# Kernel optimization log

Hardware: AMD Instinct MI355X
Metric: run time of the kernel (lower is better)

Reference implementation:

```python
import jax, jax.numpy as jnp
import numpy as np


def setup_inputs() -> dict:
    key = jax.random.key(0)
    k1, k2, k3 = jax.random.split(key, 3)
    B, C_in, C_out, T = 16, 512, 512, 4096
    pre = jax.random.normal(k1, (B, C_in, T), dtype=jnp.float32)
    # nn.Linear weight layout: [out_features, in_features]
    W_pre = jax.random.normal(k2, (C_out, C_in), dtype=jnp.float32) * (1.0 / np.sqrt(C_in))
    b_pre = jax.random.normal(k3, (C_out,), dtype=jnp.float32) * 0.01
    return {"pre": pre, "W_pre": W_pre, "b_pre": b_pre}


def reference(pre, W_pre, b_pre):
    # Original 'casual' branch loops over T applying w_pre(_pre[:,:,i]) into BOTH
    # embedding_prev and embedding_curr, then sums -> 2 * (W_pre @ pre + b).
    # Batched form: one einsum over the full sequence.
    y = jnp.einsum('bct,oc->bot', pre, W_pre) + b_pre[None, :, None]  # [B, C_out, T]
    return y + y
```

## Files before the change

### kernel.cpp

```cpp
#include <hip/hip_runtime.h>
#include <hip/hip_bf16.h>

typedef __attribute__((ext_vector_type(8))) short short8_t;
typedef __attribute__((ext_vector_type(4))) float f32x4;

#define BATCH 16
#define CIN   512
#define COUT  512
#define TT    4096
#define BK    128
#define NKT   (CIN / BK)

__device__ __forceinline__ uint pk2(float a, float b) {
    ushort lo = __builtin_bit_cast(ushort, __float2bfloat16(a));
    ushort hi = __builtin_bit_cast(ushort, __float2bfloat16(b));
    return (uint)lo | ((uint)hi << 16);
}

extern "C" __global__ __launch_bounds__(256)
void wconv(const float* __restrict__ W, ushort* __restrict__ Wb)
{
    const int i  = blockIdx.x * 256 + threadIdx.x;
    const int m  = i >> 7;
    const int k0 = (i & 127) * 4;
    const float4 v = *(const float4*)(W + (size_t)m * CIN + k0);
    const int bm = m >> 4, r = m & 15;
    const int ksg = k0 >> 5, g = (k0 >> 3) & 3, k7 = k0 & 7;
    uint2 q;
    q.x = pk2(v.x, v.y);
    q.y = pk2(v.z, v.w);
    *(uint2*)&Wb[(size_t)bm * 8192 + ksg * 512 + g * 128 + r * 8 + k7] = q;
}

template<bool WSB>
__global__ __launch_bounds__(256)
void conv2x1_gemm(const float* __restrict__ pre, const float* __restrict__ W,
                  const ushort* __restrict__ Wb,
                  const float* __restrict__ bias, float* __restrict__ out)
{
    __shared__ alignas(16) ushort LB[2][16 * 512];

    const int tid  = threadIdx.x;
    const int lane = tid & 63;
    const int wm   = tid >> 6;
    const int g    = lane >> 4;
    const int l15  = lane & 15;

    const int id   = ((blockIdx.x & 7) << 9) | (blockIdx.x >> 3);
    const int mblk = id & 3;
    const int ti   = (id >> 2) & 63;
    const int bb   = id >> 8;

    const int m0 = mblk << 7;
    const int t0 = ti << 6;

    const float* preB   = pre + (size_t)bb * ((size_t)CIN * TT);
    const int    bmBase = (m0 >> 4) + wm * 2;

    const int b_p  = tid >> 4;
    const int b_tg = tid & 15;
    const int k0   = b_p << 3;

    float4   braw[8];
    short8_t af[4][2];

    f32x4 acc[2][4];
#pragma unroll
    for (int i = 0; i < 2; ++i)
#pragma unroll
        for (int j = 0; j < 4; ++j) acc[i][j] = (f32x4)0.0f;

#define LOAD_A(KT) do { \
    if constexpr (WSB) { \
        _Pragma("unroll") \
        for (int ks = 0; ks < 4; ++ks) \
            _Pragma("unroll") \
            for (int mi = 0; mi < 2; ++mi) \
                af[ks][mi] = *(const short8_t*)(Wb + (size_t)(bmBase + mi) * 8192 \
                                                + ((KT)*4 + ks) * 512 + g * 128 + l15 * 8); \
    } else { \
        _Pragma("unroll") \
        for (int ks = 0; ks < 4; ++ks) \
            _Pragma("unroll") \
            for (int mi = 0; mi < 2; ++mi) { \
                const float* ab = W + (size_t)(m0 + wm*32 + mi*16 + l15) * CIN \
                                  + (KT)*BK + ks*32 + g*8; \
                const float4 u0 = *(const float4*)ab; \
                const float4 u1 = *(const float4*)(ab + 4); \
                uint4 qq; \
                qq.x = pk2(u0.x, u0.y); qq.y = pk2(u0.z, u0.w); \
                qq.z = pk2(u1.x, u1.y); qq.w = pk2(u1.z, u1.w); \
                af[ks][mi] = __builtin_bit_cast(short8_t, qq); \
            } \
    } } while (0)

#define LOAD_B(KT) do { \
    _Pragma("unroll") \
    for (int j = 0; j < 8; ++j) \
        braw[j] = *(const float4*)(preB + (size_t)((KT)*BK + k0 + j) * TT + t0 + 4*b_tg); \
    } while (0)

#define CVT_WRITE(BUF) do { \
    _Pragma("unroll") \
    for (int jt = 0; jt < 4; ++jt) { \
        uint4 q; \
        q.x = pk2(((const float*)&braw[0])[jt], ((const float*)&braw[1])[jt]); \
        q.y = pk2(((const float*)&braw[2])[jt], ((const float*)&braw[3])[jt]); \
        q.z = pk2(((const float*)&braw[4])[jt], ((const float*)&braw[5])[jt]); \
        q.w = pk2(((const float*)&braw[6])[jt], ((const float*)&braw[7])[jt]); \
        const int n  = 4*b_tg + jt; \
        const int np = n ^ ((n >> 3) & 7); \
        *(uint4*)&LB[BUF][b_p * 512 + np * 8] = q; \
    } } while (0)

#define COMPUTE(BUF) do { \
    _Pragma("unroll") \
    for (int ks = 0; ks < 4; ++ks) { \
        short8_t bf[4]; \
        _Pragma("unroll") \
        for (int ni = 0; ni < 4; ++ni) { \
            const int n  = ni*16 + l15; \
            const int np = n ^ ((n >> 3) & 7); \
            bf[ni] = *(const short8_t*)&LB[BUF][(ks*4 + g) * 512 + np * 8]; \
        } \
        _Pragma("unroll") \
        for (int mi = 0; mi < 2; ++mi) \
            _Pragma("unroll") \
            for (int ni = 0; ni < 4; ++ni) \
                acc[mi][ni] = __builtin_amdgcn_mfma_f32_16x16x32_bf16(af[ks][mi], bf[ni], acc[mi][ni], 0, 0, 0); \
    } } while (0)

    LOAD_B(0);
    CVT_WRITE(0);
    __syncthreads();

#pragma unroll
    for (int kt = 0; kt < NKT; ++kt) {
        LOAD_A(kt);
        if (kt + 1 < NKT) LOAD_B(kt + 1);
        if (kt & 1) COMPUTE(1); else COMPUTE(0);
        if (kt + 1 < NKT) {
            if (kt & 1) CVT_WRITE(0); else CVT_WRITE(1);
            __syncthreads();
        }
    }

    const int orow = m0 + wm*32 + g*4;
    float bv[2][4];
#pragma unroll
    for (int mi = 0; mi < 2; ++mi)
#pragma unroll
        for (int r = 0; r < 4; ++r)
            bv[mi][r] = bias[orow + mi*16 + r];

    float* outB = out + (size_t)bb * ((size_t)COUT * TT);
#pragma unroll
    for (int mi = 0; mi < 2; ++mi) {
#pragma unroll
        for (int ni = 0; ni < 4; ++ni) {
            const int t = t0 + ni*16 + l15;
#pragma unroll
            for (int r = 0; r < 4; ++r) {
                const int o = orow + mi*16 + r;
                outB[(size_t)o * TT + t] = 2.0f * (acc[mi][ni][r] + bv[mi][r]);
            }
        }
    }
}

extern "C" void kernel_launch(void* const* d_in, const int* in_sizes, int n_in,
                              void* d_out, int out_size, void* d_ws, size_t ws_size,
                              hipStream_t stream)
{
    const float* pre  = (const float*)d_in[0];
    const float* Wp   = (const float*)d_in[1];
    const float* bias = (const float*)d_in[2];
    float* out = (float*)d_out;

    const bool usews = (ws_size >= (size_t)(COUT * CIN * sizeof(ushort)));

    if (usews) {
        ushort* Wb = (ushort*)d_ws;
        hipLaunchKernelGGL(wconv, dim3(256), dim3(256), 0, stream, Wp, Wb);
        hipLaunchKernelGGL((conv2x1_gemm<true>), dim3(BATCH * 4 * 64), dim3(256), 0, stream,
                           pre, Wp, Wb, bias, out);
    } else {
        hipLaunchKernelGGL((conv2x1_gemm<false>), dim3(BATCH * 4 * 64), dim3(256), 0, stream,
                           pre, Wp, (const ushort*)nullptr, bias, out);
    }
}
```

Before: 77.96 us.

## Stage activations via direct global-to-LDS loads with triple-buffered pipeline

Replaces the register-staged activation loads with global_load_lds writes into a three-deep fp32 LDS ring. The K step shrinks to 32, and a separate bf16 conversion pass writes a double-buffered B tile. The main loop issues loads two steps ahead, using explicit vmcnt/lgkmcnt waits and raw barriers, so more memory traffic stays in flight and register pressure drops. The cost is four times as many K iterations, each with a barrier and only 8 MFMAs, and correctness depends on the hand-placed waitcnt and barrier ordering being right.

```diff
diff --git a/kernel.cpp b/kernel.cpp
--- a/kernel.cpp
+++ b/kernel.cpp
@@ -8,14 +8,19 @@
 #define CIN   512
 #define COUT  512
 #define TT    4096
-#define BK    128
-#define NKT   (CIN / BK)
+#define BKT   32
+#define NKT   16
 
 __device__ __forceinline__ uint pk2(float a, float b) {
     ushort lo = __builtin_bit_cast(ushort, __float2bfloat16(a));
     ushort hi = __builtin_bit_cast(ushort, __float2bfloat16(b));
     return (uint)lo | ((uint)hi << 16);
 }
+
+#define SCHEDB()   __builtin_amdgcn_sched_barrier(0)
+#define WAIT_VM(N) do { asm volatile("s_waitcnt vmcnt(" #N ")" ::: "memory"); SCHEDB(); } while (0)
+#define WAIT_LGKM() do { asm volatile("s_waitcnt lgkmcnt(0)" ::: "memory"); SCHEDB(); } while (0)
+#define RAW_BARRIER() do { __builtin_amdgcn_s_barrier(); SCHEDB(); } while (0)
 
 extern "C" __global__ __launch_bounds__(256)
 void wconv(const float* __restrict__ W, ushort* __restrict__ Wb)
@@ -38,11 +43,12 @@
                   const ushort* __restrict__ Wb,
                   const float* __restrict__ bias, float* __restrict__ out)
 {
-    __shared__ alignas(16) ushort LB[2][16 * 512];
+    __shared__ float  RAW[3][BKT * 64];
+    __shared__ ushort BF [2][4 * 64 * 8];
 
     const int tid  = threadIdx.x;
     const int lane = tid & 63;
-    const int wm   = tid >> 6;
+    const int wv   = tid >> 6;
     const int g    = lane >> 4;
     const int l15  = lane & 15;
 
@@ -55,14 +61,7 @@
     const int t0 = ti << 6;
 
     const float* preB   = pre + (size_t)bb * ((size_t)CIN * TT);
-    const int    bmBase = (m0 >> 4) + wm * 2;
-
-    const int b_p  = tid >> 4;
-    const int b_tg = tid & 15;
-    const int k0   = b_p << 3;
-
-    float4   braw[8];
-    short8_t af[4][2];
+    const int    bmBase = (m0 >> 4) + wv * 2;
 
     f32x4 acc[2][4];
 #pragma unroll
@@ -70,82 +69,84 @@
 #pragma unroll
         for (int j = 0; j < 4; ++j) acc[i][j] = (f32x4)0.0f;
 
-#define LOAD_A(KT) do { \
+#define STAGE(J) do { \
+    _Pragma("unroll") \
+    for (int i = 0; i < 2; ++i) { \
+        const int krow = wv*8 + i*4 + (lane >> 4); \
+        const float* gsrc = preB + (size_t)((J)*BKT + krow) * TT + t0 + ((lane & 15) << 2); \
+        float* ldst = &RAW[(J) % 3][(wv*128 + i*64 + lane) * 4]; \
+        __builtin_amdgcn_global_load_lds((const __attribute__((address_space(1))) void*)gsrc, \
+                                         (__attribute__((address_space(3))) void*)ldst, 16, 0, 0); \
+    } } while (0)
+
+#define LOAD_A(KT, AF) do { \
     if constexpr (WSB) { \
         _Pragma("unroll") \
-        for (int ks = 0; ks < 4; ++ks) \
-            _Pragma("unroll") \
-            for (int mi = 0; mi < 2; ++mi) \
-                af[ks][mi] = *(const short8_t*)(Wb + (size_t)(bmBase + mi) * 8192 \
-                                                + ((KT)*4 + ks) * 512 + g * 128 + l15 * 8); \
+        for (int mi = 0; mi < 2; ++mi) \
+            AF[mi] = *(const short8_t*)(Wb + (size_t)(bmBase + mi) * 8192 \
+                                        + (KT) * 512 + g * 128 + l15 * 8); \
     } else { \
         _Pragma("unroll") \
-        for (int ks = 0; ks < 4; ++ks) \
-            _Pragma("unroll") \
-            for (int mi = 0; mi < 2; ++mi) { \
-                const float* ab = W + (size_t)(m0 + wm*32 + mi*16 + l15) * CIN \
-                                  + (KT)*BK + ks*32 + g*8; \
-                const float4 u0 = *(const float4*)ab; \
-                const float4 u1 = *(const float4*)(ab + 4); \
-                uint4 qq; \
-                qq.x = pk2(u0.x, u0.y); qq.y = pk2(u0.z, u0.w); \
-                qq.z = pk2(u1.x, u1.y); qq.w = pk2(u1.z, u1.w); \
-                af[ks][mi] = __builtin_bit_cast(short8_t, qq); \
-            } \
+        for (int mi = 0; mi < 2; ++mi) { \
+            const float* ab = W + (size_t)(m0 + wv*32 + mi*16 + l15) * CIN + (KT)*BKT + g*8; \
+            const float4 u0 = *(const float4*)ab; \
+            const float4 u1 = *(const float4*)(ab + 4); \
+            uint4 qq; \
+            qq.x = pk2(u0.x, u0.y); qq.y = pk2(u0.z, u0.w); \
+            qq.z = pk2(u1.x, u1.y); qq.w = pk2(u1.z, u1.w); \
+            AF[mi] = __builtin_bit_cast(short8_t, qq); \
+        } \
     } } while (0)
 
-#define LOAD_B(KT) do { \
+#define CVT(J) do { \
+    const int ct = tid & 63; \
+    float f[8]; \
     _Pragma("unroll") \
     for (int j = 0; j < 8; ++j) \
-        braw[j] = *(const float4*)(preB + (size_t)((KT)*BK + k0 + j) * TT + t0 + 4*b_tg); \
+        f[j] = RAW[(J) % 3][(wv*8 + j) * 64 + ct]; \
+    uint4 q; \
+    q.x = pk2(f[0], f[1]); \
+    q.y = pk2(f[2], f[3]); \
+    q.z = pk2(f[4], f[5]); \
+    q.w = pk2(f[6], f[7]); \
+    *(uint4*)&BF[(J) & 1][wv * 512 + ct * 8] = q; \
     } while (0)
 
-#define CVT_WRITE(BUF) do { \
+#define MFMA_STEP(J, AF) do { \
+    short8_t bf[4]; \
     _Pragma("unroll") \
-    for (int jt = 0; jt < 4; ++jt) { \
-        uint4 q; \
-        q.x = pk2(((const float*)&braw[0])[jt], ((const float*)&braw[1])[jt]); \
-        q.y = pk2(((const float*)&braw[2])[jt], ((const float*)&braw[3])[jt]); \
-        q.z = pk2(((const float*)&braw[4])[jt], ((const float*)&braw[5])[jt]); \
-        q.w = pk2(((const float*)&braw[6])[jt], ((const float*)&braw[7])[jt]); \
-        const int n  = 4*b_tg + jt; \
-        const int np = n ^ ((n >> 3) & 7); \
-        *(uint4*)&LB[BUF][b_p * 512 + np * 8] = q; \
-    } } while (0)
+    for (int ni = 0; ni < 4; ++ni) \
+        bf[ni] = *(const short8_t*)&BF[(J) & 1][g * 512 + (ni*16 + l15) * 8]; \
+    _Pragma("unroll") \
+    for (int mi = 0; mi < 2; ++mi) \
+        _Pragma("unroll") \
+        for (int ni = 0; ni < 4; ++ni) \
+            acc[mi][ni] = __builtin_amdgcn_mfma_f32_16x16x32_bf16(AF[mi], bf[ni], acc[mi][ni], 0, 0, 0); \
+    } while (0)
 
-#define COMPUTE(BUF) do { \
-    _Pragma("unroll") \
-    for (int ks = 0; ks < 4; ++ks) { \
-        short8_t bf[4]; \
-        _Pragma("unroll") \
-        for (int ni = 0; ni < 4; ++ni) { \
-            const int n  = ni*16 + l15; \
-            const int np = n ^ ((n >> 3) & 7); \
-            bf[ni] = *(const short8_t*)&LB[BUF][(ks*4 + g) * 512 + np * 8]; \
-        } \
-        _Pragma("unroll") \
-        for (int mi = 0; mi < 2; ++mi) \
-            _Pragma("unroll") \
-            for (int ni = 0; ni < 4; ++ni) \
-                acc[mi][ni] = __builtin_amdgcn_mfma_f32_16x16x32_bf16(af[ks][mi], bf[ni], acc[mi][ni], 0, 0, 0); \
-    } } while (0)
-
-    LOAD_B(0);
-    CVT_WRITE(0);
-    __syncthreads();
+    STAGE(0);
+    STAGE(1);
+    WAIT_VM(2);
+    RAW_BARRIER();
+    CVT(0);
 
 #pragma unroll
     for (int kt = 0; kt < NKT; ++kt) {
-        LOAD_A(kt);
-        if (kt + 1 < NKT) LOAD_B(kt + 1);
-        if (kt & 1) COMPUTE(1); else COMPUTE(0);
-        if (kt + 1 < NKT) {
-            if (kt & 1) CVT_WRITE(0); else CVT_WRITE(1);
-            __syncthreads();
+        short8_t af[2];
+        LOAD_A(kt, af);
+        if (kt + 2 < NKT) {
+            STAGE(kt + 2);
+            WAIT_VM(2);
+        } else {
+            WAIT_VM(0);
         }
+        WAIT_LGKM();
+        RAW_BARRIER();
+        MFMA_STEP(kt, af);
+        if (kt + 1 < NKT) CVT(kt + 1);
     }
 
-    const int orow = m0 + wm*32 + g*4;
+    const int orow = m0 + wv*32 + g*4;
     float bv[2][4];
 #pragma unroll
     for (int mi = 0; mi < 2; ++mi)
@@ -177,15 +178,18 @@
     const float* bias = (const float*)d_in[2];
     float* out = (float*)d_out;
 
-    const bool usews = (ws_size >= (size_t)(COUT * CIN * sizeof(ushort)));
+    const size_t wb_bytes = (size_t)COUT * CIN * sizeof(ushort);
 
-    if (usews) {
+    const dim3 grid(BATCH * 4 * 64);
+    const dim3 block(256);
+
+    if (ws_size >= wb_bytes) {
         ushort* Wb = (ushort*)d_ws;
         hipLaunchKernelGGL(wconv, dim3(256), dim3(256), 0, stream, Wp, Wb);
-        hipLaunchKernelGGL((conv2x1_gemm<true>), dim3(BATCH * 4 * 64), dim3(256), 0, stream,
+        hipLaunchKernelGGL((conv2x1_gemm<true>), grid, block, 0, stream,
                            pre, Wp, Wb, bias, out);
     } else {
-        hipLaunchKernelGGL((conv2x1_gemm<false>), dim3(BATCH * 4 * 64), dim3(256), 0, stream,
+        hipLaunchKernelGGL((conv2x1_gemm<false>), grid, block, 0, stream,
                            pre, Wp, (const ushort*)nullptr, bias, out);
     }
 }
```

Result: slower. 81.72 us (+4.8%).
